# Performance work log

Measured on AMD Instinct MI355X. Metric: run time of the kernel, lower is better.

The kernel has to match this reference:

```python
import jax, jax.numpy as jnp
import numpy as np

B, N, C = 8, 4096, 256
HEADS = 8
DH = C // HEADS
SR = 4
EPS = 1e-5


def setup_inputs() -> dict:
    key = jax.random.key(0)
    ks = jax.random.split(key, 12)
    s = 0.02
    inp = {
        "x": jax.random.normal(ks[0], (B, N, C), dtype=jnp.float32),
        "H": 64,
        "W": 64,
        # nn.Linear weights stored torch-style [out, in]
        "q_w": jax.random.normal(ks[1], (C, C), dtype=jnp.float32) * s,
        "q_b": jax.random.normal(ks[2], (C,), dtype=jnp.float32) * s,
        "kv_w": jax.random.normal(ks[3], (2 * C, C), dtype=jnp.float32) * s,
        "kv_b": jax.random.normal(ks[4], (2 * C,), dtype=jnp.float32) * s,
        # Conv2d weight torch OIHW [C, C, SR, SR]
        "sr_w": jax.random.normal(ks[5], (C, C, SR, SR), dtype=jnp.float32) * s,
        "sr_b": jax.random.normal(ks[6], (C,), dtype=jnp.float32) * s,
        "ln_g": jnp.ones((C,), dtype=jnp.float32),
        "ln_b": jnp.zeros((C,), dtype=jnp.float32),
        "proj_w": jax.random.normal(ks[7], (C, C), dtype=jnp.float32) * s,
        "proj_b": jax.random.normal(ks[8], (C,), dtype=jnp.float32) * s,
    }
    return inp


def _layernorm(x, g, b):
    mu = jnp.mean(x, axis=-1, keepdims=True)
    var = jnp.mean(jnp.square(x - mu), axis=-1, keepdims=True)
    return (x - mu) * jax.lax.rsqrt(var + EPS) * g + b


def reference(x, H, W, q_w, q_b, kv_w, kv_b, sr_w, sr_b, ln_g, ln_b, proj_w, proj_b):
    b, n, c = x.shape
    scale = 1.0 / jnp.sqrt(jnp.float32(DH))

    # q projection -> [b, heads, n, dh]
    q = (x @ q_w.T + q_b).reshape(b, n, HEADS, DH).transpose(0, 2, 1, 3)

    # spatial reduction: conv stride=SR kernel=SR on the [b,H,W,c] image
    x_img = x.reshape(b, H, W, c)  # NHWC
    kern = jnp.transpose(sr_w, (2, 3, 1, 0))  # OIHW -> HWIO
    x_sr = jax.lax.conv_general_dilated(
        x_img, kern, window_strides=(SR, SR), padding="VALID",
        dimension_numbers=("NHWC", "HWIO", "NHWC")) + sr_b
    n_kv = (H // SR) * (W // SR)
    x_sr = x_sr.reshape(b, n_kv, c)
    x_sr = _layernorm(x_sr, ln_g, ln_b)

    # kv projection -> k, v: [b, heads, n_kv, dh]
    kv = (x_sr @ kv_w.T + kv_b).reshape(b, n_kv, 2, HEADS, DH)
    kv = kv.transpose(2, 0, 3, 1, 4)
    k, v = kv[0], kv[1]

    # attention (dropout rates are 0.0 / eval mode)
    attn = jnp.einsum("bhnd,bhmd->bhnm", q, k) * scale
    attn = jax.nn.softmax(attn, axis=-1)
    out = jnp.einsum("bhnm,bhmd->bhnd", attn, v)
    out = out.transpose(0, 2, 1, 3).reshape(b, n, c)
    return out @ proj_w.T + proj_b
```

## Files before the change

### kernel.cpp

```cpp
#include <hip/hip_runtime.h>

typedef unsigned short u16;
typedef float f32x4 __attribute__((ext_vector_type(4)));
typedef __bf16 bf16x4 __attribute__((ext_vector_type(4)));
typedef __bf16 bf16x8 __attribute__((ext_vector_type(8)));

#define B_ 8
#define N_ 4096
#define C_ 256
#define NKV 256
#define CEXP 0.25506604f

__device__ inline u16 f2bf(float f) {
    union { float f; unsigned u; } v; v.f = f;
    unsigned r = v.u + 0x7FFF + ((v.u >> 16) & 1);
    return (u16)(r >> 16);
}

__device__ inline void gload16(const void* g, void* l) {
    __builtin_amdgcn_global_load_lds(
        (const __attribute__((address_space(1))) void*)g,
        (__attribute__((address_space(3))) void*)l, 16, 0, 0);
}

__global__ __launch_bounds__(256) void prep_w(
    const float* __restrict__ qw, const float* __restrict__ kvw,
    const float* __restrict__ pw, const float* __restrict__ srw,
    u16* __restrict__ wq, u16* __restrict__ wkv, u16* __restrict__ wp, u16* __restrict__ wsr)
{
    int t = blockIdx.x * 256 + threadIdx.x;
    int stride = gridDim.x * 256;
    for (int i = t; i < 65536; i += stride) { wq[i] = f2bf(qw[i]); wp[i] = f2bf(pw[i]); }
    for (int i = t; i < 131072; i += stride) wkv[i] = f2bf(kvw[i]);
    for (int i = t; i < 1048576; i += stride) {
        int o = i >> 12, k = i & 4095;
        int ci = k & 255, khkw = k >> 8;
        wsr[i] = f2bf(srw[(size_t)(o * 256 + ci) * 16 + khkw]);
    }
}

__global__ __launch_bounds__(256) void prep_x(
    const float* __restrict__ x, u16* __restrict__ xb, u16* __restrict__ patches)
{
    size_t base = ((size_t)blockIdx.x * 256 + threadIdx.x) * 4;
    float4 v = *(const float4*)(x + base);
    ushort4 o;
    o.x = f2bf(v.x); o.y = f2bf(v.y); o.z = f2bf(v.z); o.w = f2bf(v.w);
    *(ushort4*)(xb + base) = o;
    int c = (int)(base & 255);
    int n = (int)((base >> 8) & 4095);
    int b = (int)(base >> 20);
    int hh = n >> 6, ww = n & 63;
    int p = (hh >> 2) * 16 + (ww >> 2);
    int k = ((hh & 3) * 4 + (ww & 3)) * 256 + c;
    *(ushort4*)(patches + (size_t)(b * 256 + p) * 4096 + k) = o;
}

template<int OUTMODE, bool SCALEK>
__global__ __launch_bounds__(256, 2) void gemm128(
    const u16* __restrict__ A, const u16* __restrict__ Bt,
    const float* __restrict__ bias, void* __restrict__ outp,
    int M, int Nn, int K, int kchunk)
{
    __shared__ __align__(16) u16 As[128 * 32];
    __shared__ __align__(16) u16 Bs[128 * 32];
    const int tid = threadIdx.x;
    const int bm = blockIdx.x, bn = blockIdx.y, bz = blockIdx.z;
    const int k0 = bz * kchunk;
    const int wid = tid >> 6, lane = tid & 63;
    const int wr = wid >> 1, wc = wid & 1;
    const int lrow = lane & 15, lkg = lane >> 4;

    f32x4 acc[4][4] = {};

    const int c1 = tid, c2 = tid + 256;
    const int r1 = c1 >> 2, cl1 = (c1 & 3) * 8;
    const int r2 = c2 >> 2, cl2 = (c2 & 3) * 8;
    const u16* aS1 = A  + (size_t)(bm * 128 + r1) * K + k0 + cl1;
    const u16* aS2 = A  + (size_t)(bm * 128 + r2) * K + k0 + cl2;
    const u16* bS1 = Bt + (size_t)(bn * 128 + r1) * K + k0 + cl1;
    const u16* bS2 = Bt + (size_t)(bn * 128 + r2) * K + k0 + cl2;
    u16* aD1 = As + c1 * 8;  u16* aD2 = As + c2 * 8;
    u16* bD1 = Bs + c1 * 8;  u16* bD2 = Bs + c2 * 8;

    for (int kk = 0; kk < kchunk; kk += 32) {
        gload16(aS1 + kk, aD1);
        gload16(aS2 + kk, aD2);
        gload16(bS1 + kk, bD1);
        gload16(bS2 + kk, bD2);
        __syncthreads();
        bf16x8 af[4], bff[4];
#pragma unroll
        for (int i = 0; i < 4; ++i) {
            af[i]  = *(const bf16x8*)(As + (wr * 64 + i * 16 + lrow) * 32 + lkg * 8);
            bff[i] = *(const bf16x8*)(Bs + (wc * 64 + i * 16 + lrow) * 32 + lkg * 8);
        }
#pragma unroll
        for (int i = 0; i < 4; ++i)
#pragma unroll
            for (int j = 0; j < 4; ++j)
                acc[i][j] = __builtin_amdgcn_mfma_f32_16x16x32_bf16(af[i], bff[j], acc[i][j], 0, 0, 0);
        __syncthreads();
    }

    const int row0 = bm * 128 + wr * 64;
    const int col0 = bn * 128 + wc * 64;
    if constexpr (OUTMODE == 2) {
        float* o = (float*)outp + (size_t)bz * M * Nn;
#pragma unroll
        for (int i = 0; i < 4; ++i)
#pragma unroll
            for (int j = 0; j < 4; ++j)
#pragma unroll
                for (int reg = 0; reg < 4; ++reg)
                    o[(size_t)(row0 + i * 16 + lkg * 4 + reg) * Nn + col0 + j * 16 + lrow] = acc[i][j][reg];
    } else {
#pragma unroll
        for (int j = 0; j < 4; ++j) {
            const int col = col0 + j * 16 + lrow;
            float bv = bias[col];
            float sc = 1.0f;
            if constexpr (SCALEK) { if (col < 256) sc = CEXP; }
#pragma unroll
            for (int i = 0; i < 4; ++i)
#pragma unroll
                for (int reg = 0; reg < 4; ++reg) {
                    const size_t idx = (size_t)(row0 + i * 16 + lkg * 4 + reg) * Nn + col;
                    const float val = (acc[i][j][reg] + bv) * sc;
                    if constexpr (OUTMODE == 1) ((u16*)outp)[idx] = f2bf(val);
                    else                        ((float*)outp)[idx] = val;
                }
        }
    }
}

__global__ __launch_bounds__(256) void ln_kernel(
    const float* __restrict__ part, const float* __restrict__ srb,
    const float* __restrict__ g, const float* __restrict__ bb, u16* __restrict__ out)
{
    const int row = blockIdx.x, c = threadIdx.x;
    const size_t idx = (size_t)row * 256 + c;
    float v = srb[c];
#pragma unroll
    for (int z = 0; z < 8; ++z) v += part[idx + (size_t)z * 524288];
    float s = v;
#pragma unroll
    for (int m = 1; m < 64; m <<= 1) s += __shfl_xor(s, m);
    __shared__ float red[4];
    if ((c & 63) == 0) red[c >> 6] = s;
    __syncthreads();
    float tot = red[0] + red[1] + red[2] + red[3];
    float mu = tot * (1.0f / 256.0f);
    float d = v - mu;
    float s2 = d * d;
#pragma unroll
    for (int m = 1; m < 64; m <<= 1) s2 += __shfl_xor(s2, m);
    __syncthreads();
    if ((c & 63) == 0) red[c >> 6] = s2;
    __syncthreads();
    float var = (red[0] + red[1] + red[2] + red[3]) * (1.0f / 256.0f);
    out[idx] = f2bf(d * rsqrtf(var + 1e-5f) * g[c] + bb[c]);
}

__global__ __launch_bounds__(256, 2) void attn_kernel(
    const u16* __restrict__ qbuf, const u16* __restrict__ kvbuf, u16* __restrict__ obuf)
{
    __shared__ __align__(16) u16 Ks[256 * 40];
    __shared__ __align__(16) u16 Vt[32 * 264];
    const int qt = blockIdx.x, h = blockIdx.y, b = blockIdx.z;
    const int tid = threadIdx.x;
    const int wid = tid >> 6, lane = tid & 63;
    const int lrow = lane & 15, lkg = lane >> 4;

    {
        const u16* ks = kvbuf + (size_t)(b * 256 + tid) * 512 + h * 32;
        u16* kd = Ks + tid * 40;
#pragma unroll
        for (int c = 0; c < 4; ++c)
            *(int4*)(kd + c * 8) = *(const int4*)(ks + c * 8);
    }
    {
        const u16* vs = kvbuf + (size_t)(b * 256 + tid) * 512 + 256 + h * 32;
#pragma unroll
        for (int j = 0; j < 8; ++j) {
            ushort4 vv = *(const ushort4*)(vs + j * 4);
            Vt[(j * 4 + 0) * 264 + tid] = vv.x;
            Vt[(j * 4 + 1) * 264 + tid] = vv.y;
            Vt[(j * 4 + 2) * 264 + tid] = vv.z;
            Vt[(j * 4 + 3) * 264 + tid] = vv.w;
        }
    }

    const int qcol = h * 32 + lkg * 8;
    bf16x8 qf = *(const bf16x8*)(qbuf +
        (size_t)(b * 4096 + qt * 64 + wid * 16 + lrow) * 256 + qcol);

    bf16x8 onesf = {};
    if (lrow == 0) {
#pragma unroll
        for (int e = 0; e < 8; ++e) onesf[e] = (__bf16)1.0f;
    }

    __syncthreads();

    f32x4 acc[16];
#pragma unroll
    for (int nf = 0; nf < 16; ++nf) acc[nf] = (f32x4){0.f, 0.f, 0.f, 0.f};
#pragma unroll
    for (int nf = 0; nf < 16; ++nf) {
        bf16x8 kfr = *(const bf16x8*)(Ks + (nf * 16 + lrow) * 40 + lkg * 8);
        acc[nf] = __builtin_amdgcn_mfma_f32_16x16x32_bf16(kfr, qf, acc[nf], 0, 0, 0);
    }

    bf16x8 pa8[8];
#pragma unroll
    for (int nf2 = 0; nf2 < 8; ++nf2) {
        bf16x8 pv;
#pragma unroll
        for (int half = 0; half < 2; ++half) {
#pragma unroll
            for (int r = 0; r < 4; ++r)
                pv[half * 4 + r] = (__bf16)exp2f(acc[2 * nf2 + half][r]);
        }
        pa8[nf2] = pv;
    }

    f32x4 o0 = (f32x4){0.f, 0.f, 0.f, 0.f};
    f32x4 o1 = (f32x4){0.f, 0.f, 0.f, 0.f};
    f32x4 o2 = (f32x4){0.f, 0.f, 0.f, 0.f};
#pragma unroll
    for (int nf2 = 0; nf2 < 8; ++nf2) {
        bf16x4 lo0 = *(const bf16x4*)(Vt + lrow * 264 + nf2 * 32 + lkg * 4);
        bf16x4 hi0 = *(const bf16x4*)(Vt + lrow * 264 + nf2 * 32 + 16 + lkg * 4);
        bf16x4 lo1 = *(const bf16x4*)(Vt + (16 + lrow) * 264 + nf2 * 32 + lkg * 4);
        bf16x4 hi1 = *(const bf16x4*)(Vt + (16 + lrow) * 264 + nf2 * 32 + 16 + lkg * 4);
        bf16x8 v0 = __builtin_shufflevector(lo0, hi0, 0, 1, 2, 3, 4, 5, 6, 7);
        bf16x8 v1 = __builtin_shufflevector(lo1, hi1, 0, 1, 2, 3, 4, 5, 6, 7);
        o0 = __builtin_amdgcn_mfma_f32_16x16x32_bf16(pa8[nf2], v0, o0, 0, 0, 0);
        o1 = __builtin_amdgcn_mfma_f32_16x16x32_bf16(pa8[nf2], v1, o1, 0, 0, 0);
        o2 = __builtin_amdgcn_mfma_f32_16x16x32_bf16(pa8[nf2], onesf, o2, 0, 0, 0);
    }

    float invq[4];
#pragma unroll
    for (int r = 0; r < 4; ++r)
        invq[r] = __shfl(__builtin_amdgcn_rcpf(o2[r]), lane & 48);

    const size_t obase = (size_t)(b * 4096 + qt * 64 + wid * 16);
#pragma unroll
    for (int r = 0; r < 4; ++r) {
        u16* op = obuf + (obase + lkg * 4 + r) * 256 + h * 32 + lrow;
        op[0]  = f2bf(o0[r] * invq[r]);
        op[16] = f2bf(o1[r] * invq[r]);
    }
}

extern "C" void kernel_launch(void* const* d_in, const int* in_sizes, int n_in,
                              void* d_out, int out_size, void* d_ws, size_t ws_size,
                              hipStream_t stream)
{
    (void)in_sizes; (void)n_in; (void)out_size; (void)ws_size;
    const float* x   = (const float*)d_in[0];
    const float* qw  = (const float*)d_in[3];
    const float* qb  = (const float*)d_in[4];
    const float* kvw = (const float*)d_in[5];
    const float* kvb = (const float*)d_in[6];
    const float* srw = (const float*)d_in[7];
    const float* srb = (const float*)d_in[8];
    const float* lng = (const float*)d_in[9];
    const float* lnb = (const float*)d_in[10];
    const float* pw  = (const float*)d_in[11];
    const float* pb  = (const float*)d_in[12];

    char* ws = (char*)d_ws;
    u16*   xb      = (u16*)(ws + 0);
    u16*   patches = (u16*)(ws + 16777216);
    float* part    = (float*)(ws + 33554432);
    u16*   wsr     = (u16*)(ws + 50331648);
    u16*   wqb     = (u16*)(ws + 52428800);
    u16*   wkvb    = (u16*)(ws + 52559872);
    u16*   wpb     = (u16*)(ws + 52822016);
    u16*   xsr     = (u16*)(ws + 52953088);
    u16*   kvo     = (u16*)(ws + 54001664);
    u16*   qbuf    = (u16*)d_out;

    prep_w<<<1024, 256, 0, stream>>>(qw, kvw, pw, srw, wqb, wkvb, wpb, wsr);
    prep_x<<<8192, 256, 0, stream>>>(x, xb, patches);
    gemm128<2, false><<<dim3(16, 2, 8), 256, 0, stream>>>(patches, wsr, nullptr, part, 2048, 256, 4096, 512);
    ln_kernel<<<2048, 256, 0, stream>>>(part, srb, lng, lnb, xsr);
    gemm128<1, true ><<<dim3(16, 4, 1), 256, 0, stream>>>(xsr, wkvb, kvb, kvo, 2048, 512, 256, 256);
    gemm128<1, false><<<dim3(256, 2, 1), 256, 0, stream>>>(xb, wqb, qb, qbuf, 32768, 256, 256, 256);
    attn_kernel<<<dim3(64, 8, 8), 256, 0, stream>>>(qbuf, kvo, patches);
    gemm128<0, false><<<dim3(256, 2, 1), 256, 0, stream>>>(patches, wpb, pb, d_out, 32768, 256, 256, 256);
}
```

Baseline: 104.4 us.

## Fuse Q projection into attention kernel and merge prep kernels

Computes the per-head Q tile inside the attention kernel with MFMA from bf16 x and Wq, instead of a separate GEMM writing Q to global memory. K fragment reads are permuted to match the Q accumulator layout. The two prep kernels are merged into one launch. This removes a kernel launch and the Q round trip but rereads x once per head.

```diff
diff --git a/kernel.cpp b/kernel.cpp
--- a/kernel.cpp
+++ b/kernel.cpp
@@ -23,24 +23,11 @@
         (__attribute__((address_space(3))) void*)l, 16, 0, 0);
 }
 
-__global__ __launch_bounds__(256) void prep_w(
+__global__ __launch_bounds__(256) void prep_all(
+    const float* __restrict__ x, u16* __restrict__ xb, u16* __restrict__ patches,
     const float* __restrict__ qw, const float* __restrict__ kvw,
     const float* __restrict__ pw, const float* __restrict__ srw,
-    u16* __restrict__ wq, u16* __restrict__ wkv, u16* __restrict__ wp, u16* __restrict__ wsr)
-{
-    int t = blockIdx.x * 256 + threadIdx.x;
-    int stride = gridDim.x * 256;
-    for (int i = t; i < 65536; i += stride) { wq[i] = f2bf(qw[i]); wp[i] = f2bf(pw[i]); }
-    for (int i = t; i < 131072; i += stride) wkv[i] = f2bf(kvw[i]);
-    for (int i = t; i < 1048576; i += stride) {
-        int o = i >> 12, k = i & 4095;
-        int ci = k & 255, khkw = k >> 8;
-        wsr[i] = f2bf(srw[(size_t)(o * 256 + ci) * 16 + khkw]);
-    }
-}
-
-__global__ __launch_bounds__(256) void prep_x(
-    const float* __restrict__ x, u16* __restrict__ xb, u16* __restrict__ patches)
+    u16* __restrict__ wqb, u16* __restrict__ wkv, u16* __restrict__ wp, u16* __restrict__ wsr)
 {
     size_t base = ((size_t)blockIdx.x * 256 + threadIdx.x) * 4;
     float4 v = *(const float4*)(x + base);
@@ -54,6 +41,16 @@
     int p = (hh >> 2) * 16 + (ww >> 2);
     int k = ((hh & 3) * 4 + (ww & 3)) * 256 + c;
     *(ushort4*)(patches + (size_t)(b * 256 + p) * 4096 + k) = o;
+
+    int t = blockIdx.x * 256 + threadIdx.x;
+    int stride = gridDim.x * 256;
+    for (int i = t; i < 65536; i += stride) { wqb[i] = f2bf(qw[i]); wp[i] = f2bf(pw[i]); }
+    for (int i = t; i < 131072; i += stride) wkv[i] = f2bf(kvw[i]);
+    for (int i = t; i < 1048576; i += stride) {
+        int oo = i >> 12, kk = i & 4095;
+        int ci = kk & 255, khkw = kk >> 8;
+        wsr[i] = f2bf(srw[(size_t)(oo * 256 + ci) * 16 + khkw]);
+    }
 }
 
 template<int OUTMODE, bool SCALEK>
@@ -163,7 +160,8 @@
 }
 
 __global__ __launch_bounds__(256, 2) void attn_kernel(
-    const u16* __restrict__ qbuf, const u16* __restrict__ kvbuf, u16* __restrict__ obuf)
+    const u16* __restrict__ xb, const u16* __restrict__ wq, const float* __restrict__ qb,
+    const u16* __restrict__ kvbuf, u16* __restrict__ obuf)
 {
     __shared__ __align__(16) u16 Ks[256 * 40];
     __shared__ __align__(16) u16 Vt[32 * 264];
@@ -191,9 +189,26 @@
         }
     }
 
-    const int qcol = h * 32 + lkg * 8;
-    bf16x8 qf = *(const bf16x8*)(qbuf +
-        (size_t)(b * 4096 + qt * 64 + wid * 16 + lrow) * 256 + qcol);
+    f32x4 aq0 = (f32x4){0.f, 0.f, 0.f, 0.f};
+    f32x4 aq1 = (f32x4){0.f, 0.f, 0.f, 0.f};
+    {
+        const u16* xrow = xb + (size_t)(b * 4096 + qt * 64 + wid * 16 + lrow) * 256 + lkg * 8;
+        const u16* wq0  = wq + (size_t)(h * 32 + lrow) * 256 + lkg * 8;
+        const u16* wq1  = wq0 + 16 * 256;
+#pragma unroll
+        for (int ks = 0; ks < 8; ++ks) {
+            bf16x8 xf = *(const bf16x8*)(xrow + ks * 32);
+            aq0 = __builtin_amdgcn_mfma_f32_16x16x32_bf16(*(const bf16x8*)(wq0 + ks * 32), xf, aq0, 0, 0, 0);
+            aq1 = __builtin_amdgcn_mfma_f32_16x16x32_bf16(*(const bf16x8*)(wq1 + ks * 32), xf, aq1, 0, 0, 0);
+        }
+    }
+    const float4 qb0 = *(const float4*)(qb + h * 32 + lkg * 4);
+    const float4 qb1 = *(const float4*)(qb + h * 32 + 16 + lkg * 4);
+    bf16x8 qf;
+    qf[0] = (__bf16)(aq0[0] + qb0.x); qf[1] = (__bf16)(aq0[1] + qb0.y);
+    qf[2] = (__bf16)(aq0[2] + qb0.z); qf[3] = (__bf16)(aq0[3] + qb0.w);
+    qf[4] = (__bf16)(aq1[0] + qb1.x); qf[5] = (__bf16)(aq1[1] + qb1.y);
+    qf[6] = (__bf16)(aq1[2] + qb1.z); qf[7] = (__bf16)(aq1[3] + qb1.w);
 
     bf16x8 onesf = {};
     if (lrow == 0) {
@@ -208,7 +223,9 @@
     for (int nf = 0; nf < 16; ++nf) acc[nf] = (f32x4){0.f, 0.f, 0.f, 0.f};
 #pragma unroll
     for (int nf = 0; nf < 16; ++nf) {
-        bf16x8 kfr = *(const bf16x8*)(Ks + (nf * 16 + lrow) * 40 + lkg * 8);
+        bf16x4 klo = *(const bf16x4*)(Ks + (nf * 16 + lrow) * 40 + lkg * 4);
+        bf16x4 khi = *(const bf16x4*)(Ks + (nf * 16 + lrow) * 40 + 16 + lkg * 4);
+        bf16x8 kfr = __builtin_shufflevector(klo, khi, 0, 1, 2, 3, 4, 5, 6, 7);
         acc[nf] = __builtin_amdgcn_mfma_f32_16x16x32_bf16(kfr, qf, acc[nf], 0, 0, 0);
     }
 
@@ -282,14 +299,11 @@
     u16*   wpb     = (u16*)(ws + 52822016);
     u16*   xsr     = (u16*)(ws + 52953088);
     u16*   kvo     = (u16*)(ws + 54001664);
-    u16*   qbuf    = (u16*)d_out;
-
-    prep_w<<<1024, 256, 0, stream>>>(qw, kvw, pw, srw, wqb, wkvb, wpb, wsr);
-    prep_x<<<8192, 256, 0, stream>>>(x, xb, patches);
+
+    prep_all<<<8192, 256, 0, stream>>>(x, xb, patches, qw, kvw, pw, srw, wqb, wkvb, wpb, wsr);
     gemm128<2, false><<<dim3(16, 2, 8), 256, 0, stream>>>(patches, wsr, nullptr, part, 2048, 256, 4096, 512);
     ln_kernel<<<2048, 256, 0, stream>>>(part, srb, lng, lnb, xsr);
     gemm128<1, true ><<<dim3(16, 4, 1), 256, 0, stream>>>(xsr, wkvb, kvb, kvo, 2048, 512, 256, 256);
-    gemm128<1, false><<<dim3(256, 2, 1), 256, 0, stream>>>(xb, wqb, qb, qbuf, 32768, 256, 256, 256);
-    attn_kernel<<<dim3(64, 8, 8), 256, 0, stream>>>(qbuf, kvo, patches);
+    attn_kernel<<<dim3(64, 8, 8), 256, 0, stream>>>(xb, wqb, qb, kvo, patches);
     gemm128<0, false><<<dim3(256, 2, 1), 256, 0, stream>>>(patches, wpb, pb, d_out, 32768, 256, 256, 256);
 }
```

Result: slower. 127.1 us (+21.7%).

## Fuse prep kernels and read conv patches via implicit im2col addressing

Applied to the files above, without the earlier changes.

Merges the weight and activation conversion kernels into one launch. It also drops the materialised patches buffer, so the strided conv GEMM computes im2col addresses directly from the bf16 copy of x. This removes a 16 MB scattered write and one kernel launch. The cost is more index arithmetic in the GEMM load path and less contiguous A-tile loads, since each 32-wide k slice now comes from a spatially strided row.

```diff
diff --git a/kernel.cpp b/kernel.cpp
--- a/kernel.cpp
+++ b/kernel.cpp
@@ -23,40 +23,30 @@
         (__attribute__((address_space(3))) void*)l, 16, 0, 0);
 }
 
-__global__ __launch_bounds__(256) void prep_w(
+__global__ __launch_bounds__(256) void prep_all(
+    const float* __restrict__ x, u16* __restrict__ xb,
     const float* __restrict__ qw, const float* __restrict__ kvw,
     const float* __restrict__ pw, const float* __restrict__ srw,
-    u16* __restrict__ wq, u16* __restrict__ wkv, u16* __restrict__ wp, u16* __restrict__ wsr)
-{
-    int t = blockIdx.x * 256 + threadIdx.x;
-    int stride = gridDim.x * 256;
-    for (int i = t; i < 65536; i += stride) { wq[i] = f2bf(qw[i]); wp[i] = f2bf(pw[i]); }
-    for (int i = t; i < 131072; i += stride) wkv[i] = f2bf(kvw[i]);
-    for (int i = t; i < 1048576; i += stride) {
-        int o = i >> 12, k = i & 4095;
-        int ci = k & 255, khkw = k >> 8;
-        wsr[i] = f2bf(srw[(size_t)(o * 256 + ci) * 16 + khkw]);
-    }
-}
-
-__global__ __launch_bounds__(256) void prep_x(
-    const float* __restrict__ x, u16* __restrict__ xb, u16* __restrict__ patches)
+    u16* __restrict__ wqb, u16* __restrict__ wkv, u16* __restrict__ wp, u16* __restrict__ wsr)
 {
     size_t base = ((size_t)blockIdx.x * 256 + threadIdx.x) * 4;
     float4 v = *(const float4*)(x + base);
     ushort4 o;
     o.x = f2bf(v.x); o.y = f2bf(v.y); o.z = f2bf(v.z); o.w = f2bf(v.w);
     *(ushort4*)(xb + base) = o;
-    int c = (int)(base & 255);
-    int n = (int)((base >> 8) & 4095);
-    int b = (int)(base >> 20);
-    int hh = n >> 6, ww = n & 63;
-    int p = (hh >> 2) * 16 + (ww >> 2);
-    int k = ((hh & 3) * 4 + (ww & 3)) * 256 + c;
-    *(ushort4*)(patches + (size_t)(b * 256 + p) * 4096 + k) = o;
-}
-
-template<int OUTMODE, bool SCALEK>
+
+    int t = blockIdx.x * 256 + threadIdx.x;
+    int stride = gridDim.x * 256;
+    for (int i = t; i < 65536; i += stride) { wqb[i] = f2bf(qw[i]); wp[i] = f2bf(pw[i]); }
+    for (int i = t; i < 131072; i += stride) wkv[i] = f2bf(kvw[i]);
+    for (int i = t; i < 1048576; i += stride) {
+        int oo = i >> 12, kk = i & 4095;
+        int ci = kk & 255, khkw = kk >> 8;
+        wsr[i] = f2bf(srw[(size_t)(oo * 256 + ci) * 16 + khkw]);
+    }
+}
+
+template<int OUTMODE, bool SCALEK, bool IM2COL>
 __global__ __launch_bounds__(256, 2) void gemm128(
     const u16* __restrict__ A, const u16* __restrict__ Bt,
     const float* __restrict__ bias, void* __restrict__ outp,
@@ -76,16 +66,33 @@
     const int c1 = tid, c2 = tid + 256;
     const int r1 = c1 >> 2, cl1 = (c1 & 3) * 8;
     const int r2 = c2 >> 2, cl2 = (c2 & 3) * 8;
-    const u16* aS1 = A  + (size_t)(bm * 128 + r1) * K + k0 + cl1;
-    const u16* aS2 = A  + (size_t)(bm * 128 + r2) * K + k0 + cl2;
+    const u16 *aS1, *aS2;
+    if constexpr (IM2COL) {
+        const int g1 = bm * 128 + r1, g2 = bm * 128 + r2;
+        const int b1 = g1 >> 8, p1 = g1 & 255;
+        const int b2 = g2 >> 8, p2 = g2 & 255;
+        aS1 = A + ((size_t)(b1 * 4096 + (p1 >> 4) * 256 + (p1 & 15) * 4) * 256 + cl1);
+        aS2 = A + ((size_t)(b2 * 4096 + (p2 >> 4) * 256 + (p2 & 15) * 4) * 256 + cl2);
+    } else {
+        aS1 = A + (size_t)(bm * 128 + r1) * K + k0 + cl1;
+        aS2 = A + (size_t)(bm * 128 + r2) * K + k0 + cl2;
+    }
     const u16* bS1 = Bt + (size_t)(bn * 128 + r1) * K + k0 + cl1;
     const u16* bS2 = Bt + (size_t)(bn * 128 + r2) * K + k0 + cl2;
     u16* aD1 = As + c1 * 8;  u16* aD2 = As + c2 * 8;
     u16* bD1 = Bs + c1 * 8;  u16* bD2 = Bs + c2 * 8;
 
     for (int kk = 0; kk < kchunk; kk += 32) {
-        gload16(aS1 + kk, aD1);
-        gload16(aS2 + kk, aD2);
+        int aoff;
+        if constexpr (IM2COL) {
+            const int K0 = k0 + kk;
+            const int khkw = K0 >> 8;
+            aoff = ((khkw >> 2) * 64 + (khkw & 3)) * 256 + (K0 & 255);
+        } else {
+            aoff = kk;
+        }
+        gload16(aS1 + aoff, aD1);
+        gload16(aS2 + aoff, aD2);
         gload16(bS1 + kk, bD1);
         gload16(bS2 + kk, bD2);
         __syncthreads();
@@ -274,7 +281,7 @@
 
     char* ws = (char*)d_ws;
     u16*   xb      = (u16*)(ws + 0);
-    u16*   patches = (u16*)(ws + 16777216);
+    u16*   att     = (u16*)(ws + 16777216);
     float* part    = (float*)(ws + 33554432);
     u16*   wsr     = (u16*)(ws + 50331648);
     u16*   wqb     = (u16*)(ws + 52428800);
@@ -284,12 +291,11 @@
     u16*   kvo     = (u16*)(ws + 54001664);
     u16*   qbuf    = (u16*)d_out;
 
-    prep_w<<<1024, 256, 0, stream>>>(qw, kvw, pw, srw, wqb, wkvb, wpb, wsr);
-    prep_x<<<8192, 256, 0, stream>>>(x, xb, patches);
-    gemm128<2, false><<<dim3(16, 2, 8), 256, 0, stream>>>(patches, wsr, nullptr, part, 2048, 256, 4096, 512);
+    prep_all<<<8192, 256, 0, stream>>>(x, xb, qw, kvw, pw, srw, wqb, wkvb, wpb, wsr);
+    gemm128<2, false, true ><<<dim3(16, 2, 8), 256, 0, stream>>>(xb, wsr, nullptr, part, 2048, 256, 4096, 512);
     ln_kernel<<<2048, 256, 0, stream>>>(part, srb, lng, lnb, xsr);
-    gemm128<1, true ><<<dim3(16, 4, 1), 256, 0, stream>>>(xsr, wkvb, kvb, kvo, 2048, 512, 256, 256);
-    gemm128<1, false><<<dim3(256, 2, 1), 256, 0, stream>>>(xb, wqb, qb, qbuf, 32768, 256, 256, 256);
-    attn_kernel<<<dim3(64, 8, 8), 256, 0, stream>>>(qbuf, kvo, patches);
-    gemm128<0, false><<<dim3(256, 2, 1), 256, 0, stream>>>(patches, wpb, pb, d_out, 32768, 256, 256, 256);
-}
+    gemm128<1, true,  false><<<dim3(16, 4, 1), 256, 0, stream>>>(xsr, wkvb, kvb, kvo, 2048, 512, 256, 256);
+    gemm128<1, false, false><<<dim3(256, 2, 1), 256, 0, stream>>>(xb, wqb, qb, qbuf, 32768, 256, 256, 256);
+    attn_kernel<<<dim3(64, 8, 8), 256, 0, stream>>>(qbuf, kvo, att);
+    gemm128<0, false, false><<<dim3(256, 2, 1), 256, 0, stream>>>(att, wpb, pb, d_out, 32768, 256, 256, 256);
+}
```

Measured after the change: 100.8 us. 1.04x faster.
